# Optimization experiments

Hardware: AMD Instinct MI355X
Metric: run time of the kernel (lower is better)

The kernel has to match this reference:

```python
import jax, jax.numpy as jnp
import numpy as np

DIM = 512
HEADS = 8
HEAD_DIM = DIM // HEADS
SCALE = HEAD_DIM ** -0.5
LN_EPS = 1e-5


def _layernorm(t, g, b):
    mu = jnp.mean(t, axis=-1, keepdims=True)
    var = jnp.mean(jnp.square(t - mu), axis=-1, keepdims=True)
    return (t - mu) * jax.lax.rsqrt(var + LN_EPS) * g + b


def setup_inputs() -> dict:
    key = jax.random.key(0)
    ks = jax.random.split(key, 8)
    B, C, H, W = 2, DIM, 48, 48
    s = 1.0 / np.sqrt(DIM)
    return {
        "x": jax.random.normal(ks[0], (B, C, H, W), jnp.float32),
        "y": jax.random.normal(ks[1], (B, C, H, W), jnp.float32),
        # linear weights stored [in, out]
        "k_w": jax.random.uniform(ks[2], (DIM, DIM), jnp.float32, -s, s),
        "k_b": jax.random.uniform(ks[3], (DIM,), jnp.float32, -s, s),
        "qv_w": jax.random.uniform(ks[4], (DIM, 2 * DIM), jnp.float32, -s, s),
        "qv_b": jax.random.uniform(ks[5], (2 * DIM,), jnp.float32, -s, s),
        "lnx_g": jnp.ones((DIM,), jnp.float32),
        "lnx_b": jnp.zeros((DIM,), jnp.float32),
        "lny_g": jnp.ones((DIM,), jnp.float32),
        "lny_b": jnp.zeros((DIM,), jnp.float32),
    }


def _split_qv(t, qv_w, qv_b):
    B, N, C = t.shape
    qv = (t @ qv_w + qv_b).reshape(B, N, 2, HEADS, HEAD_DIM)
    qv = jnp.transpose(qv, (2, 0, 3, 1, 4))  # [2, B, h, N, d]
    return qv[0], qv[1]


def _heads(t):
    B, N, C = t.shape
    return jnp.transpose(t.reshape(B, N, HEADS, HEAD_DIM), (0, 2, 1, 3))  # [B,h,N,d]


def reference(x, y, k_w, k_b, qv_w, qv_b, lnx_g, lnx_b, lny_g, lny_b):
    B, C = x.shape[0], x.shape[1]
    xf = _layernorm(jnp.transpose(x.reshape(B, C, -1), (0, 2, 1)), lnx_g, lnx_b)  # [B,N,C]
    yf = _layernorm(jnp.transpose(y.reshape(B, C, -1), (0, 2, 1)), lny_g, lny_b)
    N = xf.shape[1]

    y_q, y_v = _split_qv(yf, qv_w, qv_b)
    x_q, x_v = _split_qv(xf, qv_w, qv_b)
    y_k = _heads(yf @ k_w + k_b)
    x_k = _heads(xf @ k_w + k_b)

    # branch 1: softmax(x_q y_k^T) x_v  -> standard [B,N,C]
    a1 = jax.nn.softmax(jnp.einsum('bhnd,bhmd->bhnm', x_q, y_k) * SCALE, axis=-1)
    xo = jnp.einsum('bhnm,bhmd->bhnd', a1, x_v)
    xo = jnp.transpose(xo, (0, 2, 1, 3)).reshape(B, N, C)

    # branch 2: faithful reproduction of torch quirk (x_k kept a leading 1-dim,
    # so the output [1,B,h,N,d].transpose(1,2).reshape(B,N,C) scrambles layout)
    a2 = jax.nn.softmax(jnp.einsum('bhnd,bhmd->bhnm', y_q, x_k) * SCALE, axis=-1)
    yo = jnp.einsum('bhnm,bhmd->bhnd', a2, y_v)  # [B,h,N,d]
    yo = jnp.transpose(yo[None], (0, 2, 1, 3, 4)).reshape(B, N, C)

    return jnp.concatenate([xo, yo], axis=0)  # [2B, N, C]
```

## Files before the change

kernel.cpp:

```cpp
#include <hip/hip_runtime.h>

#define DIM 512
#define NTOK 2304
#define HEADS 8
#define HD 64
#define LN_EPS 1e-5f
#define BNC 2359296
#define QSC 0.18033688011112042f

typedef __attribute__((ext_vector_type(8))) short short8;
typedef __attribute__((ext_vector_type(4))) short sh4;
typedef __attribute__((ext_vector_type(4))) float f32x4;

__device__ __forceinline__ short f2bf(float f) {
    union { float f; unsigned u; } x; x.f = f;
    unsigned r = (x.u + 0x7fffu + ((x.u >> 16) & 1u)) >> 16;
    return (short)(r & 0xffffu);
}
__device__ __forceinline__ unsigned fbits(float f) {
    union { float f; unsigned u; } x; x.f = f; return x.u;
}
__device__ __forceinline__ void gl2lds(const short* g, short* l) {
    __builtin_amdgcn_global_load_lds(
        (const __attribute__((address_space(1))) unsigned int*)g,
        (__attribute__((address_space(3))) unsigned int*)l, 16, 0, 0);
}

__global__ void k_pre(const float* __restrict__ x, const float* __restrict__ y,
                      const float* __restrict__ qv_w, const float* __restrict__ k_w,
                      const float* __restrict__ qv_b, const float* __restrict__ k_b,
                      const float* __restrict__ gx, const float* __restrict__ bx,
                      const float* __restrict__ gy, const float* __restrict__ by,
                      short* __restrict__ T, short* __restrict__ Wt,
                      float* __restrict__ bias) {
    __shared__ __align__(16) float tile[64][65];
    __shared__ float pS[4][64], pQ[4][64];
    __shared__ float muL[64], rsL[64];
    int bkid = blockIdx.x, tid = threadIdx.x;
    if (bkid < 1152) {
        int nt = bkid % 36, ct = (bkid / 36) % 8, sb = bkid / 288;
        int s = sb >> 1, b = sb & 1;
        int n0 = nt * 64, c0 = ct * 64;
        const float* src = (s ? y : x) + (size_t)b * DIM * NTOK;
        int nl = tid & 63, part = tid >> 6;
        {
            const float* p = src + n0 + nl;
            float sum = 0.f, sq = 0.f;
            for (int c = part * 128; c < part * 128 + 128; c++) {
                float v = p[(size_t)c * NTOK];
                sum += v; sq += v * v;
            }
            pS[part][nl] = sum; pQ[part][nl] = sq;
        }
        __syncthreads();
        if (tid < 64) {
            float ts = pS[0][tid] + pS[1][tid] + pS[2][tid] + pS[3][tid];
            float tq = pQ[0][tid] + pQ[1][tid] + pQ[2][tid] + pQ[3][tid];
            float m = ts * (1.0f / DIM);
            float var = tq * (1.0f / DIM) - m * m;
            muL[tid] = m;
            rsL[tid] = rsqrtf(var + LN_EPS);
        }
        for (int slot = tid; slot < 1024; slot += 256) {
            int r = slot >> 4, q = slot & 15;
            const float* p = src + (size_t)(c0 + r) * NTOK + n0 + q * 4;
            float4 v = *(const float4*)p;
            tile[r][q*4+0] = v.x; tile[r][q*4+1] = v.y;
            tile[r][q*4+2] = v.z; tile[r][q*4+3] = v.w;
        }
        __syncthreads();
        const float* g  = s ? gy : gx;
        const float* be = s ? by : bx;
        int nr = tid >> 2, cg = tid & 3;
        float m = muL[nr], r_ = rsL[nr];
        short8 o0, o1;
        for (int i = 0; i < 8; i++) {
            int c = c0 + cg * 16 + i;
            o0[i] = f2bf((tile[cg*16+i][nr] - m) * r_ * g[c] + be[c]);
        }
        for (int i = 0; i < 8; i++) {
            int c = c0 + cg * 16 + 8 + i;
            o1[i] = f2bf((tile[cg*16+8+i][nr] - m) * r_ * g[c] + be[c]);
        }
        short* dst = T + ((size_t)sb * NTOK + n0 + nr) * DIM + c0 + cg * 16;
        *(short8*)dst = o0;
        *(short8*)(dst + 8) = o1;
        return;
    }
    int idx = bkid - 1152;
    int jt = idx % 24, ct = idx / 24;
    int j0 = jt * 64, c0 = ct * 64;
    if (ct == 0 && tid < 64) {
        int j = j0 + tid;
        bias[j] = (j < 1024) ? qv_b[j] : k_b[j - 1024];
    }
    for (int slot = tid; slot < 1024; slot += 256) {
        int r = slot >> 4, q = slot & 15;
        int c = c0 + r;
        float4 v;
        if (j0 < 1024) v = *(const float4*)(qv_w + (size_t)c * 1024 + j0 + q * 4);
        else           v = *(const float4*)(k_w  + (size_t)c * 512  + (j0 - 1024) + q * 4);
        tile[r][q*4+0] = v.x; tile[r][q*4+1] = v.y;
        tile[r][q*4+2] = v.z; tile[r][q*4+3] = v.w;
    }
    __syncthreads();
    int jr = tid >> 2, cg = tid & 3;
    short8 o0, o1;
    for (int i = 0; i < 8; i++) o0[i] = f2bf(tile[cg*16+i][jr]);
    for (int i = 0; i < 8; i++) o1[i] = f2bf(tile[cg*16+8+i][jr]);
    short* dst = Wt + (size_t)(j0 + jr) * DIM + c0 + cg * 16;
    *(short8*)dst = o0;
    *(short8*)(dst + 8) = o1;
}

__global__ void __launch_bounds__(256)
k_gemm(const short* __restrict__ T, const short* __restrict__ Wt,
       const float* __restrict__ bias, short* __restrict__ QVK,
       short* __restrict__ VT) {
    __shared__ __align__(16) short Abuf[2][128 * 64];
    __shared__ __align__(16) short Bbuf[2][128 * 64];
    int n0 = blockIdx.x * 128, j0 = blockIdx.y * 128, sb = blockIdx.z;
    int tid = threadIdx.x;
    int w = tid >> 6, l = tid & 63;
    int wr = w >> 1, wc = w & 1;
    int lrow = l & 15, quad = l >> 4;
    int r_in = (l >> 3) & 7, cc = l & 7;
    int ch = cc ^ r_in;
    int sw0 = (quad ^ (lrow & 7)) * 8;
    const short* Ab = T + (size_t)sb * NTOK * DIM;
    f32x4 acc[4][4] = {};

    #pragma unroll
    for (int inst = 0; inst < 4; inst++) {
        int R = w * 32 + inst * 8 + r_in;
        gl2lds(Ab + (size_t)(n0 + R) * 512 + 0 * 64 + ch * 8, &Abuf[0][(w * 32 + inst * 8) * 64]);
        gl2lds(Wt + (size_t)(j0 + R) * 512 + 0 * 64 + ch * 8, &Bbuf[0][(w * 32 + inst * 8) * 64]);
    }
    int cur = 0;
    for (int kk = 0; kk < 8; kk++) {
        __syncthreads();
        if (kk + 1 < 8) {
            #pragma unroll
            for (int inst = 0; inst < 4; inst++) {
                int R = w * 32 + inst * 8 + r_in;
                gl2lds(Ab + (size_t)(n0 + R) * 512 + (kk + 1) * 64 + ch * 8,
                       &Abuf[cur ^ 1][(w * 32 + inst * 8) * 64]);
                gl2lds(Wt + (size_t)(j0 + R) * 512 + (kk + 1) * 64 + ch * 8,
                       &Bbuf[cur ^ 1][(w * 32 + inst * 8) * 64]);
            }
        }
        #pragma unroll
        for (int c2 = 0; c2 < 2; c2++) {
            int off = c2 ? (sw0 ^ 32) : sw0;
            short8 af[4], bf[4];
            #pragma unroll
            for (int i = 0; i < 4; i++)
                af[i] = *(const short8*)&Abuf[cur][(wr*64 + i*16 + lrow) * 64 + off];
            #pragma unroll
            for (int j = 0; j < 4; j++)
                bf[j] = *(const short8*)&Bbuf[cur][(wc*64 + j*16 + lrow) * 64 + off];
            #pragma unroll
            for (int i = 0; i < 4; i++)
                #pragma unroll
                for (int j = 0; j < 4; j++)
                    acc[i][j] = __builtin_amdgcn_mfma_f32_16x16x32_bf16(bf[j], af[i], acc[i][j], 0, 0, 0);
        }
        cur ^= 1;
    }
    if (j0 >= 512 && j0 < 1024) {
        __syncthreads();
        short* sm = &Abuf[0][0];
        #pragma unroll
        for (int i = 0; i < 4; i++)
            #pragma unroll
            for (int j = 0; j < 4; j++) {
                int jb = wc * 64 + j * 16 + quad * 4;
                int nloc = wr * 64 + i * 16 + lrow;
                float4 bv4 = *(const float4*)&bias[j0 + jb];
                float bvs[4] = {bv4.x, bv4.y, bv4.z, bv4.w};
                #pragma unroll
                for (int reg = 0; reg < 4; reg++) {
                    int jloc = jb + reg;
                    sm[jloc * 128 + (((nloc >> 3) ^ (jloc & 15)) * 8) + (nloc & 7)]
                        = f2bf(acc[i][j][reg] + bvs[reg]);
                }
            }
        __syncthreads();
        for (int slot = tid; slot < 2048; slot += 256) {
            int row = slot >> 4, seg = slot & 15;
            short8 v = *(const short8*)&sm[row * 128 + ((seg ^ (row & 15)) * 8)];
            *(short8*)(VT + ((size_t)sb * 512 + (j0 - 512) + row) * NTOK + n0 + seg * 8) = v;
        }
    } else {
        #pragma unroll
        for (int i = 0; i < 4; i++) {
            int n = n0 + wr * 64 + i * 16 + lrow;
            #pragma unroll
            for (int j = 0; j < 4; j++) {
                int jjb = j0 + wc * 64 + j * 16 + quad * 4;
                float4 bv4 = *(const float4*)&bias[jjb];
                float bvs[4] = {bv4.x, bv4.y, bv4.z, bv4.w};
                float sc = (jjb < 512) ? QSC : 1.0f;
                sh4 pk;
                #pragma unroll
                for (int reg = 0; reg < 4; reg++)
                    pk[reg] = f2bf((acc[i][j][reg] + bvs[reg]) * sc);
                *(sh4*)&QVK[((size_t)sb * NTOK + n) * 1536 + jjb] = pk;
            }
        }
    }
}

__global__ void __launch_bounds__(256)
k_attn(const short* __restrict__ QVK, const short* __restrict__ VT,
       float* __restrict__ out, float* __restrict__ Opart,
       float* __restrict__ lbuf, int ntiles) {
    __shared__ __align__(16) short Kbuf[2][64 * 64];
    __shared__ __align__(16) short Vbuf[2][64 * 64];
    __shared__ __align__(16) short Qs[64 * 64];
    int id = blockIdx.x;
    int half = id / 1152;
    int rid = id % 1152;
    int xcd = rid & 7, rem = rid >> 3;
    int qt = rem % 36, yhi = rem / 36;
    int yb = yhi * 8 + xcd;
    int br = yb >> 4;
    int b  = (yb >> 3) & 1;
    int h  = yb & 7;
    int tid = threadIdx.x;
    int w = tid >> 6, l = tid & 63;
    int lrow = l & 15, quad = l >> 4;
    int r_in = (l >> 3) & 7, cc = l & 7;
    int ch = cc ^ r_in;
    int sw0 = (quad ^ (lrow & 7)) * 8;
    int n0 = qt * 64;
    int m_base = half * ntiles * 64;
    const short* Qg = QVK + ((size_t)(br * 2 + b) * NTOK) * 1536 + h * 64;
    const short* Kg = QVK + ((size_t)((1 - br) * 2 + b) * NTOK) * 1536 + 1024 + h * 64;
    const short* Vg = VT + ((size_t)(br * 2 + b) * 512 + h * 64) * NTOK;

    for (int inst = 0; inst < 2; inst++) {
        int R = w * 16 + inst * 8 + r_in;
        gl2lds(Qg + (size_t)(n0 + R) * 1536 + ch * 8, &Qs[(w * 16 + inst * 8) * 64]);
    }

    const short* KnA = Kg + (size_t)(m_base + w * 16 + r_in) * 1536 + ch * 8;
    const short* KnB = Kg + (size_t)(m_base + w * 16 + 8 + r_in) * 1536 + ch * 8;
    const short* VnA = Vg + (size_t)(w * 16 + r_in) * NTOK + m_base + ch * 8;
    const short* VnB = Vg + (size_t)(w * 16 + 8 + r_in) * NTOK + m_base + ch * 8;
    int lds_off = l * 8;

    short8 ka = *(const short8*)(KnA);
    short8 kb = *(const short8*)(KnB);
    short8 va = *(const short8*)(VnA);
    short8 vb = *(const short8*)(VnB);
    KnA += (size_t)64 * 1536; KnB += (size_t)64 * 1536;
    VnA += 64; VnB += 64;

    __syncthreads();
    short8 bq0 = *(const short8*)&Qs[(w * 16 + lrow) * 64 + sw0];
    short8 bq1 = *(const short8*)&Qs[(w * 16 + lrow) * 64 + (sw0 ^ 32)];
    short* Pw = &Qs[w * 16 * 64];

    *(short8*)&Kbuf[0][(w * 16)     * 64 + lds_off] = ka;
    *(short8*)&Kbuf[0][(w * 16 + 8) * 64 + lds_off] = kb;
    *(short8*)&Vbuf[0][(w * 16)     * 64 + lds_off] = va;
    *(short8*)&Vbuf[0][(w * 16 + 8) * 64 + lds_off] = vb;
    ka = *(const short8*)(KnA);
    kb = *(const short8*)(KnB);
    va = *(const short8*)(VnA);
    vb = *(const short8*)(VnB);
    KnA += (size_t)64 * 1536; KnB += (size_t)64 * 1536;
    VnA += 64; VnB += 64;

    short8 ones;
    for (int i = 0; i < 8; i++) ones[i] = (short)0x3F80;

    f32x4 Oacc[4] = {};
    f32x4 lacc = {};
    int cur = 0;

    for (int mt = 0; mt < ntiles; mt++) {
        __syncthreads();
        const short* Ks = Kbuf[cur];
        const short* Vs = Vbuf[cur];

        for (int sub = 0; sub < 4; sub++) {
            short8 ak0 = *(const short8*)&Ks[(sub * 16 + lrow) * 64 + sw0];
            short8 ak1 = *(const short8*)&Ks[(sub * 16 + lrow) * 64 + (sw0 ^ 32)];
            f32x4 a = {};
            __builtin_amdgcn_s_setprio(1);
            a = __builtin_amdgcn_mfma_f32_16x16x32_bf16(ak0, bq0, a, 0, 0, 0);
            a = __builtin_amdgcn_mfma_f32_16x16x32_bf16(ak1, bq1, a, 0, 0, 0);
            __builtin_amdgcn_s_setprio(0);
            float p0 = __builtin_amdgcn_exp2f(a[0]), p1 = __builtin_amdgcn_exp2f(a[1]);
            float p2 = __builtin_amdgcn_exp2f(a[2]), p3 = __builtin_amdgcn_exp2f(a[3]);
            uint2 pk;
            pk.x = __builtin_amdgcn_perm(fbits(p1), fbits(p0), 0x07060302u);
            pk.y = __builtin_amdgcn_perm(fbits(p3), fbits(p2), 0x07060302u);
            *(uint2*)&Pw[lrow * 64 + (((2 * sub + (quad >> 1)) ^ (lrow & 7)) * 8) + (quad & 1) * 4] = pk;
        }

        short8 ap0 = *(const short8*)&Pw[lrow * 64 + sw0];
        short8 ap1 = *(const short8*)&Pw[lrow * 64 + (sw0 ^ 32)];
        __builtin_amdgcn_s_setprio(1);
        lacc = __builtin_amdgcn_mfma_f32_16x16x32_bf16(ones, ap0, lacc, 0, 0, 0);
        lacc = __builtin_amdgcn_mfma_f32_16x16x32_bf16(ones, ap1, lacc, 0, 0, 0);
        for (int ddt = 0; ddt < 4; ddt++) {
            short8 av0 = *(const short8*)&Vs[(ddt * 16 + lrow) * 64 + sw0];
            short8 av1 = *(const short8*)&Vs[(ddt * 16 + lrow) * 64 + (sw0 ^ 32)];
            Oacc[ddt] = __builtin_amdgcn_mfma_f32_16x16x32_bf16(av0, ap0, Oacc[ddt], 0, 0, 0);
            Oacc[ddt] = __builtin_amdgcn_mfma_f32_16x16x32_bf16(av1, ap1, Oacc[ddt], 0, 0, 0);
        }
        __builtin_amdgcn_s_setprio(0);

        if (mt + 1 < ntiles) {
            *(short8*)&Kbuf[cur ^ 1][(w * 16)     * 64 + lds_off] = ka;
            *(short8*)&Kbuf[cur ^ 1][(w * 16 + 8) * 64 + lds_off] = kb;
            *(short8*)&Vbuf[cur ^ 1][(w * 16)     * 64 + lds_off] = va;
            *(short8*)&Vbuf[cur ^ 1][(w * 16 + 8) * 64 + lds_off] = vb;
        }
        if (mt + 2 < ntiles) {
            ka = *(const short8*)(KnA);
            kb = *(const short8*)(KnB);
            va = *(const short8*)(VnA);
            vb = *(const short8*)(VnB);
        }
        KnA += (size_t)64 * 1536; KnB += (size_t)64 * 1536;
        VnA += 64; VnB += 64;
        cur ^= 1;
    }

    int n = n0 + w * 16 + lrow;
    if (quad == 0) lbuf[half * (32 * NTOK) + yb * NTOK + n] = lacc[0];
    for (int ddt = 0; ddt < 4; ddt++) {
        float4 o;
        o.x = Oacc[ddt][0];
        o.y = Oacc[ddt][1];
        o.z = Oacc[ddt][2];
        o.w = Oacc[ddt][3];
        if (half == 0) {
            if (br == 0)
                *(float4*)&out[((size_t)b * NTOK + n) * 512 + h * 64 + ddt * 16 + quad * 4] = o;
            else
                *(float4*)&out[(size_t)BNC + ((size_t)(h * 2 + b) * NTOK + n) * 64 + ddt * 16 + quad * 4] = o;
        } else {
            *(float4*)&Opart[(size_t)(half - 1) * 4718592 +
                             ((size_t)yb * NTOK + n) * 64 + ddt * 16 + quad * 4] = o;
        }
    }
}

__global__ void __launch_bounds__(256)
k_norm(float* __restrict__ out, const float* __restrict__ Opart,
       const float* __restrict__ lbuf, int ns) {
    int i = blockIdx.x * 256 + threadIdx.x;
    int o = i * 4;
    int yb, n, d;
    if (o < BNC) {
        int b = o / (NTOK * 512);
        int r = o % (NTOK * 512);
        n = r >> 9;
        int c = r & 511;
        d = c & 63;
        yb = b * 8 + (c >> 6);
    } else {
        int o2 = o - BNC;
        int hb = o2 / (NTOK * 64);
        n = (o2 >> 6) % NTOK;
        d = o2 & 63;
        yb = 16 + (hb & 1) * 8 + (hb >> 1);
    }
    int li = yb * NTOK + n;
    float lsum = 0.f;
    for (int k = 0; k < ns; k++) lsum += lbuf[k * (32 * NTOK) + li];
    float linv = 1.f / lsum;
    float4 a = *(const float4*)&out[o];
    for (int k = 1; k < ns; k++) {
        float4 q = *(const float4*)&Opart[(size_t)(k - 1) * 4718592 + (size_t)li * 64 + d];
        a.x += q.x; a.y += q.y; a.z += q.z; a.w += q.w;
    }
    a.x *= linv; a.y *= linv; a.z *= linv; a.w *= linv;
    *(float4*)&out[o] = a;
}

extern "C" void kernel_launch(void* const* d_in, const int* in_sizes, int n_in,
                              void* d_out, int out_size, void* d_ws, size_t ws_size,
                              hipStream_t stream) {
    const float* x     = (const float*)d_in[0];
    const float* y     = (const float*)d_in[1];
    const float* k_w   = (const float*)d_in[2];
    const float* k_b   = (const float*)d_in[3];
    const float* qv_w  = (const float*)d_in[4];
    const float* qv_b  = (const float*)d_in[5];
    const float* lnx_g = (const float*)d_in[6];
    const float* lnx_b = (const float*)d_in[7];
    const float* lny_g = (const float*)d_in[8];
    const float* lny_b = (const float*)d_in[9];
    float* out = (float*)d_out;

    char* ws = (char*)d_ws;
    float* bias = (float*)ws;
    short* T    = (short*)(ws + 6144);
    short* Wt   = T + 4718592;
    short* QVK  = Wt + 786432;
    short* VT   = QVK + 14155776;
    float* lbuf = (float*)(ws + 48764928);
    float* Opart= (float*)(ws + 49944576);

    int ns = (ws_size >= 49944576ull + 3ull * 18874368ull) ? 4
           : (ws_size >= 49944576ull + 1ull * 18874368ull) ? 2 : 2;
    int ntiles = 36 / ns;

    k_pre  <<<1344, 256, 0, stream>>>(x, y, qv_w, k_w, qv_b, k_b,
                                      lnx_g, lnx_b, lny_g, lny_b, T, Wt, bias);
    k_gemm <<<dim3(18, 12, 4), 256, 0, stream>>>(T, Wt, bias, QVK, VT);
    k_attn <<<1152 * ns, 256, 0, stream>>>(QVK, VT, out, Opart, lbuf, ntiles);
    k_norm <<<4608, 256, 0, stream>>>(out, Opart, lbuf, ns);
}
```

Measured before the change: 210.2 us.

## Double query tile per attention block to reuse K/V tiles across 128 rows

Each attention workgroup now handles 128 query rows instead of 64, with each wave computing two 16-row query sub-blocks against every K/V tile loaded into LDS. This halves the number of blocks and the K/V global traffic per query row, and raises MFMA work per LDS read of K and V. It also removes the setprio hints and fully unrolls the inner loops. In exchange it doubles the accumulator register footprint, grows the Q LDS buffer, and leaves fewer blocks to fill the device.

```diff
diff --git a/kernel.cpp b/kernel.cpp
--- a/kernel.cpp
+++ b/kernel.cpp
@@ -217,12 +217,12 @@
        float* __restrict__ lbuf, int ntiles) {
     __shared__ __align__(16) short Kbuf[2][64 * 64];
     __shared__ __align__(16) short Vbuf[2][64 * 64];
-    __shared__ __align__(16) short Qs[64 * 64];
+    __shared__ __align__(16) short Qs[128 * 64];
     int id = blockIdx.x;
-    int half = id / 1152;
-    int rid = id % 1152;
+    int half = id / 576;
+    int rid = id % 576;
     int xcd = rid & 7, rem = rid >> 3;
-    int qt = rem % 36, yhi = rem / 36;
+    int qt = rem % 18, yhi = rem / 18;
     int yb = yhi * 8 + xcd;
     int br = yb >> 4;
     int b  = (yb >> 3) & 1;
@@ -233,15 +233,16 @@
     int r_in = (l >> 3) & 7, cc = l & 7;
     int ch = cc ^ r_in;
     int sw0 = (quad ^ (lrow & 7)) * 8;
-    int n0 = qt * 64;
+    int n0 = qt * 128;
     int m_base = half * ntiles * 64;
     const short* Qg = QVK + ((size_t)(br * 2 + b) * NTOK) * 1536 + h * 64;
     const short* Kg = QVK + ((size_t)((1 - br) * 2 + b) * NTOK) * 1536 + 1024 + h * 64;
     const short* Vg = VT + ((size_t)(br * 2 + b) * 512 + h * 64) * NTOK;
 
-    for (int inst = 0; inst < 2; inst++) {
-        int R = w * 16 + inst * 8 + r_in;
-        gl2lds(Qg + (size_t)(n0 + R) * 1536 + ch * 8, &Qs[(w * 16 + inst * 8) * 64]);
+    #pragma unroll
+    for (int j = 0; j < 4; j++) {
+        int R = w * 32 + j * 8 + r_in;
+        gl2lds(Qg + (size_t)(n0 + R) * 1536 + ch * 8, &Qs[(w * 32 + j * 8) * 64]);
     }
 
     const short* KnA = Kg + (size_t)(m_base + w * 16 + r_in) * 1536 + ch * 8;
@@ -258,9 +259,13 @@
     VnA += 64; VnB += 64;
 
     __syncthreads();
-    short8 bq0 = *(const short8*)&Qs[(w * 16 + lrow) * 64 + sw0];
-    short8 bq1 = *(const short8*)&Qs[(w * 16 + lrow) * 64 + (sw0 ^ 32)];
-    short* Pw = &Qs[w * 16 * 64];
+    short8 bq[2][2];
+    #pragma unroll
+    for (int qb = 0; qb < 2; qb++) {
+        bq[qb][0] = *(const short8*)&Qs[(w * 32 + qb * 16 + lrow) * 64 + sw0];
+        bq[qb][1] = *(const short8*)&Qs[(w * 32 + qb * 16 + lrow) * 64 + (sw0 ^ 32)];
+    }
+    short* Pw = &Qs[(w * 32) * 64];
 
     *(short8*)&Kbuf[0][(w * 16)     * 64 + lds_off] = ka;
     *(short8*)&Kbuf[0][(w * 16 + 8) * 64 + lds_off] = kb;
@@ -274,10 +279,11 @@
     VnA += 64; VnB += 64;
 
     short8 ones;
+    #pragma unroll
     for (int i = 0; i < 8; i++) ones[i] = (short)0x3F80;
 
-    f32x4 Oacc[4] = {};
-    f32x4 lacc = {};
+    f32x4 Oacc[2][4] = {};
+    f32x4 lacc[2] = {};
     int cur = 0;
 
     for (int mt = 0; mt < ntiles; mt++) {
@@ -285,34 +291,43 @@
         const short* Ks = Kbuf[cur];
         const short* Vs = Vbuf[cur];
 
+        #pragma unroll
         for (int sub = 0; sub < 4; sub++) {
             short8 ak0 = *(const short8*)&Ks[(sub * 16 + lrow) * 64 + sw0];
             short8 ak1 = *(const short8*)&Ks[(sub * 16 + lrow) * 64 + (sw0 ^ 32)];
-            f32x4 a = {};
-            __builtin_amdgcn_s_setprio(1);
-            a = __builtin_amdgcn_mfma_f32_16x16x32_bf16(ak0, bq0, a, 0, 0, 0);
-            a = __builtin_amdgcn_mfma_f32_16x16x32_bf16(ak1, bq1, a, 0, 0, 0);
-            __builtin_amdgcn_s_setprio(0);
-            float p0 = __builtin_amdgcn_exp2f(a[0]), p1 = __builtin_amdgcn_exp2f(a[1]);
-            float p2 = __builtin_amdgcn_exp2f(a[2]), p3 = __builtin_amdgcn_exp2f(a[3]);
-            uint2 pk;
-            pk.x = __builtin_amdgcn_perm(fbits(p1), fbits(p0), 0x07060302u);
-            pk.y = __builtin_amdgcn_perm(fbits(p3), fbits(p2), 0x07060302u);
-            *(uint2*)&Pw[lrow * 64 + (((2 * sub + (quad >> 1)) ^ (lrow & 7)) * 8) + (quad & 1) * 4] = pk;
-        }
-
-        short8 ap0 = *(const short8*)&Pw[lrow * 64 + sw0];
-        short8 ap1 = *(const short8*)&Pw[lrow * 64 + (sw0 ^ 32)];
-        __builtin_amdgcn_s_setprio(1);
-        lacc = __builtin_amdgcn_mfma_f32_16x16x32_bf16(ones, ap0, lacc, 0, 0, 0);
-        lacc = __builtin_amdgcn_mfma_f32_16x16x32_bf16(ones, ap1, lacc, 0, 0, 0);
+            #pragma unroll
+            for (int qb = 0; qb < 2; qb++) {
+                f32x4 a = {};
+                a = __builtin_amdgcn_mfma_f32_16x16x32_bf16(ak0, bq[qb][0], a, 0, 0, 0);
+                a = __builtin_amdgcn_mfma_f32_16x16x32_bf16(ak1, bq[qb][1], a, 0, 0, 0);
+                float p0 = __builtin_amdgcn_exp2f(a[0]), p1 = __builtin_amdgcn_exp2f(a[1]);
+                float p2 = __builtin_amdgcn_exp2f(a[2]), p3 = __builtin_amdgcn_exp2f(a[3]);
+                uint2 pk;
+                pk.x = __builtin_amdgcn_perm(fbits(p1), fbits(p0), 0x07060302u);
+                pk.y = __builtin_amdgcn_perm(fbits(p3), fbits(p2), 0x07060302u);
+                *(uint2*)&Pw[(qb * 16 + lrow) * 64 +
+                             (((2 * sub + (quad >> 1)) ^ (lrow & 7)) * 8) + (quad & 1) * 4] = pk;
+            }
+        }
+
+        short8 ap[2][2];
+        #pragma unroll
+        for (int qb = 0; qb < 2; qb++) {
+            ap[qb][0] = *(const short8*)&Pw[(qb * 16 + lrow) * 64 + sw0];
+            ap[qb][1] = *(const short8*)&Pw[(qb * 16 + lrow) * 64 + (sw0 ^ 32)];
+            lacc[qb] = __builtin_amdgcn_mfma_f32_16x16x32_bf16(ones, ap[qb][0], lacc[qb], 0, 0, 0);
+            lacc[qb] = __builtin_amdgcn_mfma_f32_16x16x32_bf16(ones, ap[qb][1], lacc[qb], 0, 0, 0);
+        }
+        #pragma unroll
         for (int ddt = 0; ddt < 4; ddt++) {
             short8 av0 = *(const short8*)&Vs[(ddt * 16 + lrow) * 64 + sw0];
             short8 av1 = *(const short8*)&Vs[(ddt * 16 + lrow) * 64 + (sw0 ^ 32)];
-            Oacc[ddt] = __builtin_amdgcn_mfma_f32_16x16x32_bf16(av0, ap0, Oacc[ddt], 0, 0, 0);
-            Oacc[ddt] = __builtin_amdgcn_mfma_f32_16x16x32_bf16(av1, ap1, Oacc[ddt], 0, 0, 0);
-        }
-        __builtin_amdgcn_s_setprio(0);
+            #pragma unroll
+            for (int qb = 0; qb < 2; qb++) {
+                Oacc[qb][ddt] = __builtin_amdgcn_mfma_f32_16x16x32_bf16(av0, ap[qb][0], Oacc[qb][ddt], 0, 0, 0);
+                Oacc[qb][ddt] = __builtin_amdgcn_mfma_f32_16x16x32_bf16(av1, ap[qb][1], Oacc[qb][ddt], 0, 0, 0);
+            }
+        }
 
         if (mt + 1 < ntiles) {
             *(short8*)&Kbuf[cur ^ 1][(w * 16)     * 64 + lds_off] = ka;
@@ -331,22 +346,26 @@
         cur ^= 1;
     }
 
-    int n = n0 + w * 16 + lrow;
-    if (quad == 0) lbuf[half * (32 * NTOK) + yb * NTOK + n] = lacc[0];
-    for (int ddt = 0; ddt < 4; ddt++) {
-        float4 o;
-        o.x = Oacc[ddt][0];
-        o.y = Oacc[ddt][1];
-        o.z = Oacc[ddt][2];
-        o.w = Oacc[ddt][3];
-        if (half == 0) {
-            if (br == 0)
-                *(float4*)&out[((size_t)b * NTOK + n) * 512 + h * 64 + ddt * 16 + quad * 4] = o;
-            else
-                *(float4*)&out[(size_t)BNC + ((size_t)(h * 2 + b) * NTOK + n) * 64 + ddt * 16 + quad * 4] = o;
-        } else {
-            *(float4*)&Opart[(size_t)(half - 1) * 4718592 +
-                             ((size_t)yb * NTOK + n) * 64 + ddt * 16 + quad * 4] = o;
+    #pragma unroll
+    for (int qb = 0; qb < 2; qb++) {
+        int n = n0 + w * 32 + qb * 16 + lrow;
+        if (quad == 0) lbuf[half * (32 * NTOK) + yb * NTOK + n] = lacc[qb][0];
+        #pragma unroll
+        for (int ddt = 0; ddt < 4; ddt++) {
+            float4 o;
+            o.x = Oacc[qb][ddt][0];
+            o.y = Oacc[qb][ddt][1];
+            o.z = Oacc[qb][ddt][2];
+            o.w = Oacc[qb][ddt][3];
+            if (half == 0) {
+                if (br == 0)
+                    *(float4*)&out[((size_t)b * NTOK + n) * 512 + h * 64 + ddt * 16 + quad * 4] = o;
+                else
+                    *(float4*)&out[(size_t)BNC + ((size_t)(h * 2 + b) * NTOK + n) * 64 + ddt * 16 + quad * 4] = o;
+            } else {
+                *(float4*)&Opart[(size_t)(half - 1) * 4718592 +
+                                 ((size_t)yb * NTOK + n) * 64 + ddt * 16 + quad * 4] = o;
+            }
         }
     }
 }
@@ -409,12 +428,12 @@
     float* Opart= (float*)(ws + 49944576);
 
     int ns = (ws_size >= 49944576ull + 3ull * 18874368ull) ? 4
-           : (ws_size >= 49944576ull + 1ull * 18874368ull) ? 2 : 2;
+           : 2;
     int ntiles = 36 / ns;
 
     k_pre  <<<1344, 256, 0, stream>>>(x, y, qv_w, k_w, qv_b, k_b,
                                       lnx_g, lnx_b, lny_g, lny_b, T, Wt, bias);
     k_gemm <<<dim3(18, 12, 4), 256, 0, stream>>>(T, Wt, bias, QVK, VT);
-    k_attn <<<1152 * ns, 256, 0, stream>>>(QVK, VT, out, Opart, lbuf, ntiles);
+    k_attn <<<576 * ns, 256, 0, stream>>>(QVK, VT, out, Opart, lbuf, ntiles);
     k_norm <<<4608, 256, 0, stream>>>(out, Opart, lbuf, ns);
 }
```

Result: faster. 201.8 us (-4.0%).
